# Kernel tuning notes

Measured on AMD Instinct MI355X. Metric: run time of the kernel, lower is better.

Reference implementation:

```python
import jax, jax.numpy as jnp
import numpy as np

LIS_DIM = 256
LIS_LAYERS = 3
MAX_FRAMES = 1700
MEL_DIM = 40
PET_BOOL = True
REP = 2 * LIS_DIM
B = 32
T = 1696
SCI_FACTOR = float(np.sqrt(REP / MEL_DIM)) * 20.0


def _pet():
    # sinusoidal positional encoding, exactly as Listener.compute_pet
    pos = np.arange(MAX_FRAMES, dtype=np.float64)
    d = np.arange(REP)
    ang = pos[:, None] / (10000.0 ** ((d // 2 * 2) / REP))[None, :]
    pet = np.where(d % 2 == 0, np.sin(ang), np.cos(ang)).astype(np.float32)
    return jnp.asarray(pet * np.float32(PET_BOOL))


def _lstm(x, mask, Wk, Wr, b):
    # Keras-semantics masked LSTM. x: [B,T,D], mask: [B,T] bool -> [B,T,U].
    # Gate order i, f, g(c), o as in Keras. Masked steps carry h,c (and output h).
    xz = jnp.einsum('btd,dh->bth', x, Wk) + b  # precompute input projection
    U = Wr.shape[0]

    def step(carry, inp):
        h, c = carry
        zx, m = inp  # zx: [B,4U], m: [B]
        z = zx + h @ Wr
        i, f, g, o = jnp.split(z, 4, axis=-1)
        c_new = jax.nn.sigmoid(f) * c + jax.nn.sigmoid(i) * jnp.tanh(g)
        h_new = jax.nn.sigmoid(o) * jnp.tanh(c_new)
        m = m[:, None]
        h = jnp.where(m, h_new, h)
        c = jnp.where(m, c_new, c)
        return (h, c), h

    init = (jnp.zeros((x.shape[0], U), x.dtype), jnp.zeros((x.shape[0], U), x.dtype))
    _, hs = jax.lax.scan(step, init, (xz.transpose(1, 0, 2), mask.T))
    return hs.transpose(1, 0, 2)


def _bilstm(x, mask, fk, fr, fb, bk, br, bb):
    # Keras Bidirectional(merge_mode='concat'): backward runs on time-reversed
    # input+mask, output re-reversed.
    hf = _lstm(x, mask, fk, fr, fb)
    hb = _lstm(x[:, ::-1], mask[:, ::-1], bk, br, bb)[:, ::-1]
    return jnp.concatenate([hf, hb], axis=-1)


def _forward(inputs, scale, dem_w, dem_b, layer_params, final_params, mask):
    pet = _pet()
    x = inputs @ dem_w + dem_b                       # [B,T,512]
    x = x * SCI_FACTOR * scale[0] + pet[: inputs.shape[1]]
    m = mask
    for fk, fr, fb, bk, br, bb in layer_params:
        x = _bilstm(x, m, fk, fr, fb, bk, br, bb)    # [B,t,512]
        Bb, Tt, D = x.shape
        x = x.reshape(Bb, Tt // 2, 2 * D)            # pyramid: halve time
        m = jnp.all(m.reshape(Bb, Tt // 2, 2), axis=-1)
    h = _bilstm(x, m, *final_params)                 # [B,T/8,512]
    return h, m


def setup_inputs():
    key = jax.random.key(0)
    ks = jax.random.split(key, 40)

    def w(k, shape):
        return (jax.random.normal(k, shape) * 0.08).astype(jnp.float32)

    inp = {}
    inp['inputs'] = jax.random.normal(ks[0], (B, T, MEL_DIM), jnp.float32)
    lengths = jax.random.randint(ks[1], (B,), T // 2, T + 1)
    inp['mask'] = jnp.arange(T)[None, :] < lengths[:, None]
    inp['scale'] = jnp.array([0.05], jnp.float32)
    inp['dem_w'] = w(ks[2], (MEL_DIM, REP))
    inp['dem_b'] = jnp.zeros((REP,), jnp.float32)
    dims = [REP, 4 * LIS_DIM, 4 * LIS_DIM]
    ki = 3
    for i, din in enumerate(dims):
        for pre in ('fw', 'bw'):
            inp[f'l{i}_{pre}_k'] = w(ks[ki], (din, 4 * LIS_DIM)); ki += 1
            inp[f'l{i}_{pre}_r'] = w(ks[ki], (LIS_DIM, 4 * LIS_DIM)); ki += 1
            inp[f'l{i}_{pre}_b'] = jnp.zeros((4 * LIS_DIM,), jnp.float32)
    for pre in ('fw', 'bw'):
        inp[f'f_{pre}_k'] = w(ks[ki], (4 * LIS_DIM, 4 * LIS_DIM)); ki += 1
        inp[f'f_{pre}_r'] = w(ks[ki], (LIS_DIM, 4 * LIS_DIM)); ki += 1
        inp[f'f_{pre}_b'] = jnp.zeros((4 * LIS_DIM,), jnp.float32)
    return inp


def reference(inputs, scale, dem_w, dem_b,
              l0_fw_k, l0_fw_r, l0_fw_b, l0_bw_k, l0_bw_r, l0_bw_b,
              l1_fw_k, l1_fw_r, l1_fw_b, l1_bw_k, l1_bw_r, l1_bw_b,
              l2_fw_k, l2_fw_r, l2_fw_b, l2_bw_k, l2_bw_r, l2_bw_b,
              f_fw_k, f_fw_r, f_fw_b, f_bw_k, f_bw_r, f_bw_b,
              mask):
    layer_params = [
        (l0_fw_k, l0_fw_r, l0_fw_b, l0_bw_k, l0_bw_r, l0_bw_b),
        (l1_fw_k, l1_fw_r, l1_fw_b, l1_bw_k, l1_bw_r, l1_bw_b),
        (l2_fw_k, l2_fw_r, l2_fw_b, l2_bw_k, l2_bw_r, l2_bw_b),
    ]
    final_params = (f_fw_k, f_fw_r, f_fw_b, f_bw_k, f_bw_r, f_bw_b)
    return _forward(inputs, scale, dem_w, dem_b, layer_params, final_params, mask)
```

## Files before the change

### kernel.cpp

```cpp
#include <hip/hip_runtime.h>

typedef unsigned int u32;
typedef unsigned short u16;
typedef unsigned long long u64;
typedef __attribute__((ext_vector_type(8))) short bf16x8;
typedef __attribute__((ext_vector_type(4))) float f32x4;
typedef __attribute__((ext_vector_type(4))) unsigned int u32x4;

#define MFMA16(a, b, c) __builtin_amdgcn_mfma_f32_16x16x32_bf16((a), (b), (c), 0, 0, 0)

__device__ __forceinline__ float bf2f(u16 h) {
  union { u32 u; float f; } x; x.u = ((u32)h) << 16; return x.f;
}
__device__ __forceinline__ u16 f2bf(float f) {
  union { float f; u32 u; } x; x.f = f;
  u32 r = (x.u + 0x7FFFu + ((x.u >> 16) & 1u)) >> 16;
  return (u16)r;
}
__device__ __forceinline__ float sigm(float x) { return 1.0f / (1.0f + __expf(-x)); }
__device__ __forceinline__ float tanh_(float x) {
  float e = __expf(2.0f * x);
  return 1.0f - 2.0f / (e + 1.0f);
}

__device__ __forceinline__ bool flags8_plain(const u32* p, u32 tag) {
  u32x4 a, b;
  asm volatile("global_load_dwordx4 %0, %2, off\n\t"
               "global_load_dwordx4 %1, %2, off offset:16\n\t"
               "s_waitcnt vmcnt(0)"
               : "=&v"(a), "=&v"(b) : "v"(p) : "memory");
  return (a.x == tag) & (a.y == tag) & (a.z == tag) & (a.w == tag) &
         (b.x == tag) & (b.y == tag) & (b.z == tag) & (b.w == tag);
}
__device__ __forceinline__ bool flags8_agent(const u32* p, u32 tag) {
  const u64 want = (u64)tag * 0x0000000100000001ULL;
  bool ok = true;
#pragma unroll
  for (int i = 0; i < 4; ++i)
    ok &= (__hip_atomic_load((const u64*)p + i, __ATOMIC_RELAXED,
                             __HIP_MEMORY_SCOPE_AGENT) == want);
  return ok;
}
__device__ __forceinline__ u32x4 ld16_agent(const u32* p) {
  u64 a = __hip_atomic_load((const u64*)p, __ATOMIC_RELAXED, __HIP_MEMORY_SCOPE_AGENT);
  u64 b = __hip_atomic_load((const u64*)(p + 2), __ATOMIC_RELAXED, __HIP_MEMORY_SCOPE_AGENT);
  return (u32x4){(u32)a, (u32)(a >> 32), (u32)b, (u32)(b >> 32)};
}

__global__ void sentinelK(float* __restrict__ out) {
  if (threadIdx.x == 0) out[0] = 1.0e6f;
}

__global__ void modeK(const unsigned char* __restrict__ m, int* __restrict__ mode) {
  if (threadIdx.x == 0) *mode = (m[1] | m[2]) ? 1 : 4;
}

__device__ __forceinline__ bool rawmask(const void* mp, int md, int b, int t) {
  if (md == 1) return ((const unsigned char*)mp)[b * 1696 + t] != 0;
  return ((const int*)mp)[b * 1696 + t] != 0;
}

__global__ __launch_bounds__(256) void maskK(
    const void* __restrict__ m, const int* __restrict__ mode,
    unsigned char* __restrict__ m0, unsigned char* __restrict__ m1,
    unsigned char* __restrict__ m2, unsigned char* __restrict__ m3,
    float* __restrict__ outMask) {
  int idx = blockIdx.x * 256 + threadIdx.x;
  int t = idx >> 5, b = idx & 31;
  int md = *mode;
  m0[t * 32 + b] = rawmask(m, md, b, t) ? 1 : 0;
  if (t < 848) {
    bool a = rawmask(m, md, b, 2 * t) && rawmask(m, md, b, 2 * t + 1);
    m1[t * 32 + b] = a ? 1 : 0;
  }
  if (t < 424) {
    bool a = true;
    for (int j = 0; j < 4; ++j) a = a && rawmask(m, md, b, 4 * t + j);
    m2[t * 32 + b] = a ? 1 : 0;
  }
  if (t < 212) {
    bool a = true;
    for (int j = 0; j < 8; ++j) a = a && rawmask(m, md, b, 8 * t + j);
    m3[t * 32 + b] = a ? 1 : 0;
    outMask[b * 212 + t] = a ? 1.0f : 0.0f;
  }
}

__global__ __launch_bounds__(256) void petK(float* __restrict__ pet) {
  int idx = blockIdx.x * 256 + threadIdx.x;
  int t = idx >> 9, d = idx & 511;
  double e = (double)((d >> 1) * 2) / 512.0;
  double freq = exp(e * -9.210340371976184);
  double ang = (double)t * freq;
  double vv = (d & 1) ? cos(ang) : sin(ang);
  pet[idx] = (float)vv;
}

__global__ __launch_bounds__(256) void packW(const float* __restrict__ src,
                                             u16* __restrict__ dst, int ksh, int N) {
  int idx = blockIdx.x * 256 + threadIdx.x;
  int n = idx >> ksh;
  int k = idx & ((1 << ksh) - 1);
  dst[idx] = f2bf(src[(size_t)k * N + n]);
}

__global__ void biasK(const float* __restrict__ fb, const float* __restrict__ bb,
                      float* __restrict__ dst) {
  int i = blockIdx.x * 256 + threadIdx.x;
  dst[i] = (i < 1024) ? fb[i] : bb[i - 1024];
}

__global__ __launch_bounds__(256) void x0cK(
    const float* __restrict__ inp, const float* __restrict__ dw,
    const float* __restrict__ db, const float* __restrict__ scale,
    const float* __restrict__ pet, u16* __restrict__ xc,
    int t0f, int t0b, int Cl) {
  const int bid = blockIdx.x;
  const int d = (bid >= Cl) ? 1 : 0;
  const int lt = bid - d * Cl;
  const int t = (d ? t0b : t0f) + lt;
  __shared__ float xin[32][40];
  for (int i = threadIdx.x; i < 1280; i += 256) {
    int b = i / 40, k = i - b * 40;
    xin[b][k] = inp[((size_t)b * 1696 + t) * 40 + k];
  }
  __syncthreads();
  const float sc = 71.554175279993267f * scale[0];
  for (int dd = threadIdx.x; dd < 512; dd += 256) {
    float w[40];
#pragma unroll
    for (int k = 0; k < 40; ++k) w[k] = dw[k * 512 + dd];
    const float pv = pet[t * 512 + dd];
    const float bv = db[dd];
    u16* out = xc + (((size_t)d * Cl + lt) * 32) * 512 + dd;
    for (int b = 0; b < 32; ++b) {
      float acc = bv;
#pragma unroll
      for (int k = 0; k < 40; ++k) acc += xin[b][k] * w[k];
      out[(size_t)b * 512] = f2bf(acc * sc + pv);
    }
  }
}

__device__ __forceinline__ void gemm_tile(
    u16* As, u16* Bs,
    const u16* Af, const u16* Ab, const u16* Wp, const float* bias,
    float* out, int K, int Cl, int bm, int bn, int d, int tid) {
  const u16* A = (d ? Ab : Af) + (size_t)bm * 128 * K;
  const u16* W = Wp + (size_t)d * (size_t)K * 1024 + (size_t)bn * 128 * K;
  const int wv = tid >> 6, L = tid & 63, ln = L & 15, q = L >> 4;
  const int wm = wv & 1, wn = wv >> 1;
  const int srow = L >> 3, scol = (L & 7) * 8;

  f32x4 acc[4][4];
#pragma unroll
  for (int mt = 0; mt < 4; ++mt)
#pragma unroll
    for (int nt = 0; nt < 4; ++nt) acc[mt][nt] = (f32x4){0.f, 0.f, 0.f, 0.f};

  for (int kt = 0; kt < K; kt += 64) {
#pragma unroll
    for (int j = 0; j < 4; ++j) {
      const int rg = (j * 4 + wv) * 8;
      const u16* gA = A + (size_t)(rg + srow) * K + kt + scol;
      const u16* gB = W + (size_t)(rg + srow) * K + kt + scol;
      __builtin_amdgcn_global_load_lds(
          (const __attribute__((address_space(1))) void*)gA,
          (__attribute__((address_space(3))) void*)&As[rg * 64], 16, 0, 0);
      __builtin_amdgcn_global_load_lds(
          (const __attribute__((address_space(1))) void*)gB,
          (__attribute__((address_space(3))) void*)&Bs[rg * 64], 16, 0, 0);
    }
    __syncthreads();
#pragma unroll
    for (int ks = 0; ks < 2; ++ks) {
      bf16x8 a[4], b[4];
#pragma unroll
      for (int mt = 0; mt < 4; ++mt)
        a[mt] = *(const bf16x8*)&As[(wm * 64 + mt * 16 + ln) * 64 + ks * 32 + q * 8];
#pragma unroll
      for (int nt = 0; nt < 4; ++nt)
        b[nt] = *(const bf16x8*)&Bs[(wn * 64 + nt * 16 + ln) * 64 + ks * 32 + q * 8];
#pragma unroll
      for (int mt = 0; mt < 4; ++mt)
#pragma unroll
        for (int nt = 0; nt < 4; ++nt) acc[mt][nt] = MFMA16(a[mt], b[nt], acc[mt][nt]);
    }
    __syncthreads();
  }

  float* outd = out + (size_t)d * Cl * 32768;
#pragma unroll
  for (int nt = 0; nt < 4; ++nt) {
    const int col = bn * 128 + wn * 64 + nt * 16 + ln;
    const float bv = bias[d * 1024 + col];
#pragma unroll
    for (int mt = 0; mt < 4; ++mt) {
      const int row0 = bm * 128 + wm * 64 + mt * 16 + q * 4;
#pragma unroll
      for (int r = 0; r < 4; ++r)
        outd[(size_t)(row0 + r) * 1024 + col] = acc[mt][nt][r] + bv;
    }
  }
}

__global__ __launch_bounds__(256) void gemmK(
    const u16* __restrict__ Af, const u16* __restrict__ Ab,
    const u16* __restrict__ Wp, const float* __restrict__ bias,
    float* __restrict__ out, int K, int Cl) {
  __shared__ u16 As[128 * 64];
  __shared__ u16 Bs[128 * 64];
  gemm_tile(As, Bs, Af, Ab, Wp, bias, out, K, Cl,
            blockIdx.x, blockIdx.y, blockIdx.z, threadIdx.x);
}

__global__ __launch_bounds__(256) void fusedK(
    const float* __restrict__ xzR,
    const u16* __restrict__ WrP,
    u16* __restrict__ hbufS,
    float* __restrict__ cbufL,
    int* __restrict__ flagsS,
    const unsigned char* __restrict__ msk,
    u16* __restrict__ Xnext,
    float* __restrict__ outH,
    int T, int Cl, int s0, int isFinal,
    const u16* __restrict__ Af2, const u16* __restrict__ Ab2,
    const u16* __restrict__ WpK, const float* __restrict__ biasL,
    float* __restrict__ xzW, int Kg, int Cg,
    int* __restrict__ doneL, int doneVal, int tagBase) {
  __shared__ u16 As[128 * 64];
  __shared__ u16 Bs[128 * 64];
  __shared__ u16 A_lds[32 * 264];
  __shared__ int hdone;
  __shared__ int sh_fasti;
  const int bid = blockIdx.x;
  const int tid = threadIdx.x;
  const int sub = bid & 7;
  const int grp = bid >> 3;

  if (sub == 0 && grp < 16) {
    const int rid = grp;
    const int dir = rid >> 3;
    const int wg = rid & 7;
    const int v = tid >> 6;
    const int L = tid & 63;
    const int ln = L & 15;
    const int q = L >> 4;
    const bool low = (L & 8) == 0;
    const int ug = wg * 32 + v * 8 + (L & 7);

    u32* ringB = (u32*)flagsS + dir * 128;
    u32* ringM = (u32*)flagsS + 1024 + dir * 4096;

    if (tid == 0) {
      u32 xcc = (u32)__builtin_amdgcn_s_getreg(63508) & 0xFu;
      int* chk = flagsS + 256 + ((tagBase >> 8) << 2);
      __hip_atomic_fetch_or(&chk[dir], (int)(1u << xcc), __ATOMIC_RELAXED,
                            __HIP_MEMORY_SCOPE_AGENT);
      __hip_atomic_fetch_add(&chk[2 + dir], 1, __ATOMIC_RELAXED,
                             __HIP_MEMORY_SCOPE_AGENT);
      int spins = 0;
      while (__hip_atomic_load(&chk[2 + dir], __ATOMIC_RELAXED,
                               __HIP_MEMORY_SCOPE_AGENT) < 8) {
        __builtin_amdgcn_s_sleep(2);
        if (++spins > (1 << 20)) {
          __hip_atomic_fetch_or(&chk[dir], 0x7FFFFFFF, __ATOMIC_RELAXED,
                                __HIP_MEMORY_SCOPE_AGENT);
          break;
        }
      }
      int om = __hip_atomic_load(&chk[dir], __ATOMIC_RELAXED,
                                 __HIP_MEMORY_SCOPE_AGENT);
      sh_fasti = (__popc((u32)om) == 1) ? 1 : 0;
    }
    __syncthreads();
    const bool fastp = (sh_fasti != 0);

    bf16x8 bfr[2][8];
    {
      const u16* wr = WrP + (size_t)dir * 262144;
#pragma unroll
      for (int nt = 0; nt < 2; ++nt) {
        const int n = (nt * 2 + (ln >> 3)) * 256 + ug;
#pragma unroll
        for (int ks = 0; ks < 8; ++ks)
          bfr[nt][ks] = *(const bf16x8*)(wr + (size_t)n * 256 + ks * 32 + q * 8);
      }
    }
    u16* hb = hbufS + dir * 32768;
    float* cb = cbufL + dir * 8192;

    float cst[2][4];
    if (s0 == 0) {
#pragma unroll
      for (int mt = 0; mt < 2; ++mt)
#pragma unroll
        for (int r = 0; r < 4; ++r) cst[mt][r] = 0.f;
    } else {
#pragma unroll
      for (int mt = 0; mt < 2; ++mt)
#pragma unroll
        for (int r = 0; r < 4; ++r)
          cst[mt][r] = cb[(mt * 16 + q * 4 + r) * 256 + ug];
    }

    for (int s = s0; s < s0 + Cl; ++s) {
      const int t = dir ? (T - 1 - s) : s;
      const int lt = dir ? (s0 + Cl - 1 - s) : (s - s0);
      const int ls = s - s0;

      float xzv[2][2][4];
      const float* xzt = xzR + ((size_t)dir * Cl + lt) * 32768;
#pragma unroll
      for (int nt = 0; nt < 2; ++nt) {
        const int ncol = (nt * 2 + (ln >> 3)) * 256 + ug;
#pragma unroll
        for (int mt = 0; mt < 2; ++mt)
#pragma unroll
          for (int r = 0; r < 4; ++r)
            xzv[mt][nt][r] = xzt[(size_t)(mt * 16 + q * 4 + r) * 1024 + ncol];
      }
      const u32 mk0 = *(const u32*)&msk[t * 32 + q * 4];
      const u32 mk1 = *(const u32*)&msk[t * 32 + 16 + q * 4];

      if (ls > 0) {
        if (tid == 0) {
          const u32 tg = (u32)(tagBase + ls);
          const u32* fb = ringB + ((ls - 1) & 15) * 8;
          bool got = false;
          if (fastp) {
            const u32* fm = ringM + ((ls - 1) & 31) * 128;
            for (int j = 0; j < 8; ++j) {
              if (flags8_plain(fm + j * 16, tg)) { got = true; break; }
            }
          }
          if (!got) {
            int spins = 0;
            while (!flags8_agent(fb, tg)) {
              __builtin_amdgcn_s_sleep(1);
              if (++spins > (1 << 21)) break;
            }
          }
        }
        __syncthreads();
      }

      {
        const u32* hsrc = (const u32*)(hb + ((s + 3) & 3) * 8192);
        const int m0 = tid >> 5;
        const int c4 = (tid & 31) * 4;
        const u32* p0 = hsrc + (m0)*128 + c4;
        const u32* p1 = hsrc + (8 + m0) * 128 + c4;
        const u32* p2 = hsrc + (16 + m0) * 128 + c4;
        const u32* p3 = hsrc + (24 + m0) * 128 + c4;
        u32x4 v0, v1, v2, v3;
        if (fastp) {
          v0 = *(const u32x4*)p0; v1 = *(const u32x4*)p1;
          v2 = *(const u32x4*)p2; v3 = *(const u32x4*)p3;
        } else {
          v0 = ld16_agent(p0); v1 = ld16_agent(p1);
          v2 = ld16_agent(p2); v3 = ld16_agent(p3);
        }
        const int lb = (tid & 31) * 8;
        *(u32x4*)&A_lds[(m0)*264 + lb] = v0;
        *(u32x4*)&A_lds[(8 + m0) * 264 + lb] = v1;
        *(u32x4*)&A_lds[(16 + m0) * 264 + lb] = v2;
        *(u32x4*)&A_lds[(24 + m0) * 264 + lb] = v3;
      }
      __syncthreads();

      f32x4 acc[2][2];
#pragma unroll
      for (int mt = 0; mt < 2; ++mt)
#pragma unroll
        for (int nt = 0; nt < 2; ++nt) acc[mt][nt] = (f32x4){0.f, 0.f, 0.f, 0.f};
#pragma unroll
      for (int ks = 0; ks < 8; ++ks) {
        bf16x8 a0 = *(const bf16x8*)&A_lds[ln * 264 + ks * 32 + q * 8];
        bf16x8 a1 = *(const bf16x8*)&A_lds[(16 + ln) * 264 + ks * 32 + q * 8];
        acc[0][0] = MFMA16(a0, bfr[0][ks], acc[0][0]);
        acc[0][1] = MFMA16(a0, bfr[1][ks], acc[0][1]);
        acc[1][0] = MFMA16(a1, bfr[0][ks], acc[1][0]);
        acc[1][1] = MFMA16(a1, bfr[1][ks], acc[1][1]);
      }

      float hsv[2][4];
#pragma unroll
      for (int mt = 0; mt < 2; ++mt) {
        const u32 mkw = mt ? mk1 : mk0;
#pragma unroll
        for (int r = 0; r < 4; ++r) {
          float z0 = acc[mt][0][r] + xzv[mt][0][r];
          float z1 = acc[mt][1][r] + xzv[mt][1][r];
          float z0p = __shfl_xor(z0, 8);
          float z1p = __shfl_xor(z1, 8);
          float iv = low ? z0 : z0p;
          float fv = low ? z0p : z0;
          float gv = low ? z1 : z1p;
          float ov = low ? z1p : z1;
          float cold = cst[mt][r];
          float cn = sigm(fv) * cold + sigm(iv) * tanh_(gv);
          float hn = sigm(ov) * tanh_(cn);
          const int m = mt * 16 + q * 4 + r;
          float hold = bf2f(A_lds[m * 264 + ug]);
          bool mb = ((mkw >> (8 * r)) & 0xffu) != 0;
          cst[mt][r] = mb ? cn : cold;
          float hs = mb ? hn : hold;
          hsv[mt][r] = hs;
        }
      }

      {
        u32* hdst = (u32*)(hb + (s & 3) * 8192);
#pragma unroll
        for (int mt = 0; mt < 2; ++mt) {
#pragma unroll
          for (int r = 0; r < 4; ++r) {
            u32 lo = (u32)f2bf(hsv[mt][r]);
            u32 par = (u32)__shfl_xor((int)lo, 1);
            u32 val = lo | (par << 16);
            if (low && ((ln & 1) == 0)) {
              const int m = mt * 16 + q * 4 + r;
              if (fastp)
                hdst[m * 128 + (ug >> 1)] = val;
              else
                __hip_atomic_store(&hdst[m * 128 + (ug >> 1)], val,
                                   __ATOMIC_RELAXED, __HIP_MEMORY_SCOPE_AGENT);
            }
          }
        }
      }

      asm volatile("s_waitcnt vmcnt(0)" ::: "memory");
      __syncthreads();
      if (tid == 0) {
        const u32 tg = (u32)(tagBase + ls + 1);
        if (fastp) {
          u32* mir = ringM + (ls & 31) * 128 + wg;
#pragma unroll
          for (int j = 0; j < 8; ++j)
            asm volatile("global_store_dword %0, %1, off" ::"v"(mir + j * 16),
                         "v"(tg) : "memory");
        }
        __hip_atomic_store(ringB + (ls & 15) * 8 + wg, tg, __ATOMIC_RELAXED,
                           __HIP_MEMORY_SCOPE_AGENT);
      }

      if (low) {
#pragma unroll
        for (int mt = 0; mt < 2; ++mt)
#pragma unroll
          for (int r = 0; r < 4; ++r) {
            const int m = mt * 16 + q * 4 + r;
            if (isFinal)
              outH[((size_t)m * T + t) * 512 + dir * 256 + ug] = hsv[mt][r];
            else
              Xnext[((size_t)(t >> 1) * 32 + m) * 1024 + (t & 1) * 512 + dir * 256 + ug] =
                  f2bf(hsv[mt][r]);
          }
      }
    }

    if (low) {
#pragma unroll
      for (int mt = 0; mt < 2; ++mt)
#pragma unroll
        for (int r = 0; r < 4; ++r)
          cb[(mt * 16 + q * 4 + r) * 256 + ug] = cst[mt][r];
    }
    if (wg == 0 && tid == 0)
      __hip_atomic_store(&doneL[dir * 16], doneVal, __ATOMIC_RELAXED,
                         __HIP_MEMORY_SCOPE_AGENT);
  } else {
    const int gidx = (bid < 128) ? (grp * 7 + sub - 1) : (112 + (bid - 128));
    if (Cg > 0) {
      const int nM = Cg >> 2;
      const int total = nM * 16;
      for (int tt = gidx; tt < total; tt += 240) {
        const int d = tt / (nM * 8);
        const int r2 = tt - d * (nM * 8);
        const int bn = r2 / nM;
        const int bm = r2 - bn * nM;
        gemm_tile(As, Bs, Af2, Ab2, WpK, biasL, xzW, Kg, Cg, bm, bn, d, tid);
      }
    }
    if (tid == 0) hdone = 0;
    __syncthreads();
    float hx = 1.0f + (float)tid * 1.0e-6f;
    const float ha = 1.0000001f, hc = 1.0e-7f;
    for (int it = 0; it < (1 << 16); ++it) {
#pragma unroll 64
      for (int i = 0; i < 512; ++i)
        asm volatile("v_fmac_f32 %0, %1, %2" : "+v"(hx) : "v"(ha), "v"(hc));
      if (tid == 0) {
        int d0 = __hip_atomic_load(&doneL[0],  __ATOMIC_RELAXED, __HIP_MEMORY_SCOPE_AGENT);
        int d1 = __hip_atomic_load(&doneL[16], __ATOMIC_RELAXED, __HIP_MEMORY_SCOPE_AGENT);
        if (d0 >= doneVal && d1 >= doneVal) hdone = 1;
      }
      __syncthreads();
      if (hdone) break;
      __syncthreads();
    }
    if (hx == 1.2345e-37f) ((volatile float*)doneL)[8] = hx;
  }
}

extern "C" void kernel_launch(void* const* d_in, const int* in_sizes, int n_in,
                              void* d_out, int out_size, void* d_ws, size_t ws_size,
                              hipStream_t stream) {
  char* ws = (char*)d_ws;
  constexpr size_t O_PET   = 0;
  constexpr size_t O_WK    = 3473408;
  constexpr size_t O_BIAS  = O_WK + 14680064;
  constexpr size_t O_WR    = O_BIAS + 32768;
  constexpr size_t O_M0    = O_WR + 4194304;
  constexpr size_t O_M1    = O_M0 + 54272;
  constexpr size_t O_M2    = O_M1 + 27136;
  constexpr size_t O_M3    = O_M2 + 13568;
  constexpr size_t O_MODE  = O_M3 + 6784;
  constexpr size_t O_FLAGS = O_MODE + 256;
  constexpr size_t O_DONE  = O_FLAGS + 54272;
  constexpr size_t O_HBUF  = O_DONE + 512;
  constexpr size_t O_CBUF  = O_HBUF + 262144;
  constexpr size_t O_XB0   = O_CBUF + 262144;
  constexpr size_t O_XB1   = O_XB0 + 55574528;
  constexpr size_t O_XC    = O_XB1 + 27787264;

  int C = 0;
  if      (ws_size >= O_XC + 212ull * 589824) C = 212;
  else if (ws_size >= O_XC + 106ull * 589824) C = 106;
  else if (ws_size >= O_XC + 53ull * 589824)  C = 53;
  if (C == 0) { sentinelK<<<1, 64, 0, stream>>>((float*)d_out); return; }

  hipMemsetAsync(ws + O_FLAGS, 0, 54272 + 512 + 131072, stream);

  modeK<<<1, 64, 0, stream>>>((const unsigned char*)d_in[1], (int*)(ws + O_MODE));
  maskK<<<212, 256, 0, stream>>>(d_in[1], (const int*)(ws + O_MODE),
                                 (unsigned char*)(ws + O_M0), (unsigned char*)(ws + O_M1),
                                 (unsigned char*)(ws + O_M2), (unsigned char*)(ws + O_M3),
                                 (float*)d_out + 3473408);
  petK<<<3392, 256, 0, stream>>>((float*)(ws + O_PET));

  u16* wk = (u16*)(ws + O_WK);
  u16* wrp = (u16*)(ws + O_WR);
  float* bias = (float*)(ws + O_BIAS);
  packW<<<2048, 256, 0, stream>>>((const float*)d_in[5],  wk + 0,       9, 1024);
  packW<<<2048, 256, 0, stream>>>((const float*)d_in[8],  wk + 524288,  9, 1024);
  packW<<<4096, 256, 0, stream>>>((const float*)d_in[11], wk + 1048576, 10, 1024);
  packW<<<4096, 256, 0, stream>>>((const float*)d_in[14], wk + 2097152, 10, 1024);
  packW<<<4096, 256, 0, stream>>>((const float*)d_in[17], wk + 3145728, 10, 1024);
  packW<<<4096, 256, 0, stream>>>((const float*)d_in[20], wk + 4194304, 10, 1024);
  packW<<<4096, 256, 0, stream>>>((const float*)d_in[23], wk + 5242880, 10, 1024);
  packW<<<4096, 256, 0, stream>>>((const float*)d_in[26], wk + 6291456, 10, 1024);
  packW<<<1024, 256, 0, stream>>>((const float*)d_in[6],  wrp + 0,       8, 1024);
  packW<<<1024, 256, 0, stream>>>((const float*)d_in[9],  wrp + 262144,  8, 1024);
  packW<<<1024, 256, 0, stream>>>((const float*)d_in[12], wrp + 524288,  8, 1024);
  packW<<<1024, 256, 0, stream>>>((const float*)d_in[15], wrp + 786432,  8, 1024);
  packW<<<1024, 256, 0, stream>>>((const float*)d_in[18], wrp + 1048576, 8, 1024);
  packW<<<1024, 256, 0, stream>>>((const float*)d_in[21], wrp + 1310720, 8, 1024);
  packW<<<1024, 256, 0, stream>>>((const float*)d_in[24], wrp + 1572864, 8, 1024);
  packW<<<1024, 256, 0, stream>>>((const float*)d_in[27], wrp + 1835008, 8, 1024);
  biasK<<<8, 256, 0, stream>>>((const float*)d_in[7],  (const float*)d_in[10], bias + 0);
  biasK<<<8, 256, 0, stream>>>((const float*)d_in[13], (const float*)d_in[16], bias + 2048);
  biasK<<<8, 256, 0, stream>>>((const float*)d_in[19], (const float*)d_in[22], bias + 4096);
  biasK<<<8, 256, 0, stream>>>((const float*)d_in[25], (const float*)d_in[28], bias + 6144);

  u16* XB0 = (u16*)(ws + O_XB0);
  u16* XB1 = (u16*)(ws + O_XB1);
  u16* xc  = (u16*)(ws + O_XC);
  float* xzp[2] = {(float*)(ws + O_XC + (size_t)C * 65536),
                   (float*)(ws + O_XC + (size_t)C * 65536 + (size_t)C * 262144)};
  int* flags = (int*)(ws + O_FLAGS);
  int* done  = (int*)(ws + O_DONE);
  u16* hbuf = (u16*)(ws + O_HBUF);
  float* cbuf = (float*)(ws + O_CBUF);
  unsigned char* masks[4] = {
      (unsigned char*)(ws + O_M0), (unsigned char*)(ws + O_M1),
      (unsigned char*)(ws + O_M2), (unsigned char*)(ws + O_M3)};

  const int    Ts[4]    = {1696, 848, 424, 212};
  const int    Ks[4]    = {512, 1024, 1024, 1024};
  const size_t wkOff[4] = {0, 1048576, 3145728, 5242880};
  const size_t wrOff[4] = {0, 524288, 1048576, 1572864};
  const int    bOff[4]  = {0, 2048, 4096, 6144};
  u16* Xin[4]  = {nullptr, XB0, XB1, XB0};
  u16* Xout[4] = {XB0, XB1, XB0, nullptr};

  int launchIdx = 0;
  for (int l = 0; l < 4; ++l) {
    const int T = Ts[l], K = Ks[l];
    const int Cl = (C < T) ? C : T;
    const int R = T / Cl;

    if (l > 0)
      hipMemsetAsync(ws + O_HBUF, 0, 131072, stream);

    const u16 *Af, *Ab;
    if (l == 0) {
      x0cK<<<2 * Cl, 256, 0, stream>>>((const float*)d_in[0], (const float*)d_in[3],
                                       (const float*)d_in[4], (const float*)d_in[2],
                                       (const float*)(ws + O_PET), xc, 0, T - Cl, Cl);
      Af = xc; Ab = xc + (size_t)Cl * 16384;
    } else {
      Af = Xin[l]; Ab = Xin[l] + (size_t)(T - Cl) * 32768;
    }
    gemmK<<<dim3(Cl / 4, 8, 2), 256, 0, stream>>>(
        Af, Ab, wk + wkOff[l], bias + bOff[l], xzp[0], K, Cl);

    for (int r = 0; r < R; ++r) {
      const int hasN = (r + 1 < R);
      const u16 *Af2 = nullptr, *Ab2 = nullptr;
      if (hasN) {
        if (l == 0) {
          x0cK<<<2 * Cl, 256, 0, stream>>>((const float*)d_in[0], (const float*)d_in[3],
                                           (const float*)d_in[4], (const float*)d_in[2],
                                           (const float*)(ws + O_PET), xc,
                                           (r + 1) * Cl, T - (r + 2) * Cl, Cl);
          Af2 = xc; Ab2 = xc + (size_t)Cl * 16384;
        } else {
          Af2 = Xin[l] + (size_t)(r + 1) * Cl * 32768;
          Ab2 = Xin[l] + (size_t)(T - (r + 2) * Cl) * 32768;
        }
      }
      fusedK<<<256, 256, 0, stream>>>(
          xzp[r & 1], wrp + wrOff[l], hbuf,
          cbuf + (size_t)l * 16384, flags, masks[l], Xout[l],
          (l == 3) ? (float*)d_out : nullptr, T, Cl, r * Cl, (l == 3) ? 1 : 0,
          Af2, Ab2, wk + wkOff[l], bias + bOff[l], xzp[(r + 1) & 1], K,
          hasN ? Cl : 0, done + (size_t)l * 32, r + 1, launchIdx << 8);
      ++launchIdx;
    }
  }
}
```

Before: 12.82 ms.

## Halve recurrent LSTM workgroups per direction and read h directly into MFMA fragments

The recurrent part of the fused kernel now uses 4 workgroups per direction instead of 8. Each workgroup owns 64 hidden units and all four gates, which removes the cross-lane shuffles used for gate exchange and cuts the per-step inter-workgroup flag polling. The previous hidden state is loaded straight from global memory into MFMA A-fragments, skipping the LDS staging copy and one barrier. The next step's xz and mask values are prefetched into double-buffered registers, and output stores are shifted onto waves 1-3. The cost is twice as much recurrent weight held in registers per thread, more per-workgroup compute on the serial path, and a relocated mirror flag ring inside the h buffer.

```diff
diff --git a/kernel.cpp b/kernel.cpp
--- a/kernel.cpp
+++ b/kernel.cpp
@@ -23,20 +23,17 @@
   return 1.0f - 2.0f / (e + 1.0f);
 }
 
-__device__ __forceinline__ bool flags8_plain(const u32* p, u32 tag) {
-  u32x4 a, b;
-  asm volatile("global_load_dwordx4 %0, %2, off\n\t"
-               "global_load_dwordx4 %1, %2, off offset:16\n\t"
-               "s_waitcnt vmcnt(0)"
-               : "=&v"(a), "=&v"(b) : "v"(p) : "memory");
-  return (a.x == tag) & (a.y == tag) & (a.z == tag) & (a.w == tag) &
-         (b.x == tag) & (b.y == tag) & (b.z == tag) & (b.w == tag);
-}
-__device__ __forceinline__ bool flags8_agent(const u32* p, u32 tag) {
+__device__ __forceinline__ bool probe4(const u32* p, u32 tag) {
+  u32x4 a;
+  asm volatile("global_load_dwordx4 %0, %1, off\n\ts_waitcnt vmcnt(0)"
+               : "=&v"(a) : "v"(p) : "memory");
+  return (a.x == tag) & (a.y == tag) & (a.z == tag) & (a.w == tag);
+}
+__device__ __forceinline__ bool flags4_agent(const u32* p, u32 tag) {
   const u64 want = (u64)tag * 0x0000000100000001ULL;
   bool ok = true;
 #pragma unroll
-  for (int i = 0; i < 4; ++i)
+  for (int i = 0; i < 2; ++i)
     ok &= (__hip_atomic_load((const u64*)p + i, __ATOMIC_RELAXED,
                              __HIP_MEMORY_SCOPE_AGENT) == want);
   return ok;
@@ -230,7 +227,7 @@
     int* __restrict__ doneL, int doneVal, int tagBase) {
   __shared__ u16 As[128 * 64];
   __shared__ u16 Bs[128 * 64];
-  __shared__ u16 A_lds[32 * 264];
+  __shared__ float w0h[64][8];
   __shared__ int hdone;
   __shared__ int sh_fasti;
   const int bid = blockIdx.x;
@@ -238,30 +235,29 @@
   const int sub = bid & 7;
   const int grp = bid >> 3;
 
-  if (sub == 0 && grp < 16) {
+  if (sub == 0 && grp < 8) {
     const int rid = grp;
-    const int dir = rid >> 3;
-    const int wg = rid & 7;
+    const int dir = rid >> 2;
+    const int wg = rid & 3;
     const int v = tid >> 6;
     const int L = tid & 63;
     const int ln = L & 15;
     const int q = L >> 4;
-    const bool low = (L & 8) == 0;
-    const int ug = wg * 32 + v * 8 + (L & 7);
-
-    u32* ringB = (u32*)flagsS + dir * 128;
-    u32* ringM = (u32*)flagsS + 1024 + dir * 4096;
+    const int ug = wg * 64 + v * 16 + ln;
+
+    u32* ringB = (u32*)flagsS + dir * 64;
+    u32* ringM = (u32*)(hbufS + 65536) + dir * 8192;
 
     if (tid == 0) {
       u32 xcc = (u32)__builtin_amdgcn_s_getreg(63508) & 0xFu;
-      int* chk = flagsS + 256 + ((tagBase >> 8) << 2);
+      int* chk = flagsS + 128 + ((tagBase >> 8) << 2);
       __hip_atomic_fetch_or(&chk[dir], (int)(1u << xcc), __ATOMIC_RELAXED,
                             __HIP_MEMORY_SCOPE_AGENT);
       __hip_atomic_fetch_add(&chk[2 + dir], 1, __ATOMIC_RELAXED,
                              __HIP_MEMORY_SCOPE_AGENT);
       int spins = 0;
       while (__hip_atomic_load(&chk[2 + dir], __ATOMIC_RELAXED,
-                               __HIP_MEMORY_SCOPE_AGENT) < 8) {
+                               __HIP_MEMORY_SCOPE_AGENT) < 4) {
         __builtin_amdgcn_s_sleep(2);
         if (++spins > (1 << 20)) {
           __hip_atomic_fetch_or(&chk[dir], 0x7FFFFFFF, __ATOMIC_RELAXED,
@@ -276,12 +272,12 @@
     __syncthreads();
     const bool fastp = (sh_fasti != 0);
 
-    bf16x8 bfr[2][8];
+    bf16x8 bfr[4][8];
     {
       const u16* wr = WrP + (size_t)dir * 262144;
 #pragma unroll
-      for (int nt = 0; nt < 2; ++nt) {
-        const int n = (nt * 2 + (ln >> 3)) * 256 + ug;
+      for (int nt = 0; nt < 4; ++nt) {
+        const int n = nt * 256 + ug;
 #pragma unroll
         for (int ks = 0; ks < 8; ++ks)
           bfr[nt][ks] = *(const bf16x8*)(wr + (size_t)n * 256 + ks * 32 + q * 8);
@@ -304,39 +300,43 @@
           cst[mt][r] = cb[(mt * 16 + q * 4 + r) * 256 + ug];
     }
 
-    for (int s = s0; s < s0 + Cl; ++s) {
+    float xzA[2][4][4], xzB[2][4][4];
+    u32 mkA0, mkA1, mkB0, mkB1;
+
+    auto prefetch = [&](int ss, float (&xz)[2][4][4], u32& k0, u32& k1) {
+      const int ssc = (ss < s0 + Cl) ? ss : (s0 + Cl - 1);
+      const int tt = dir ? (T - 1 - ssc) : ssc;
+      const int ltt = dir ? (s0 + Cl - 1 - ssc) : (ssc - s0);
+      const float* xzt = xzR + ((size_t)dir * Cl + ltt) * 32768;
+#pragma unroll
+      for (int nt = 0; nt < 4; ++nt)
+#pragma unroll
+        for (int mt = 0; mt < 2; ++mt)
+#pragma unroll
+          for (int r = 0; r < 4; ++r)
+            xz[mt][nt][r] = xzt[(size_t)(mt * 16 + q * 4 + r) * 1024 + nt * 256 + ug];
+      k0 = *(const u32*)&msk[tt * 32 + q * 4];
+      k1 = *(const u32*)&msk[tt * 32 + 16 + q * 4];
+    };
+
+    auto step = [&](int s, float (&xzC)[2][4][4], u32 mkC0, u32 mkC1,
+                    float (&xzN)[2][4][4], u32& mkN0, u32& mkN1) {
       const int t = dir ? (T - 1 - s) : s;
-      const int lt = dir ? (s0 + Cl - 1 - s) : (s - s0);
       const int ls = s - s0;
-
-      float xzv[2][2][4];
-      const float* xzt = xzR + ((size_t)dir * Cl + lt) * 32768;
-#pragma unroll
-      for (int nt = 0; nt < 2; ++nt) {
-        const int ncol = (nt * 2 + (ln >> 3)) * 256 + ug;
-#pragma unroll
-        for (int mt = 0; mt < 2; ++mt)
-#pragma unroll
-          for (int r = 0; r < 4; ++r)
-            xzv[mt][nt][r] = xzt[(size_t)(mt * 16 + q * 4 + r) * 1024 + ncol];
-      }
-      const u32 mk0 = *(const u32*)&msk[t * 32 + q * 4];
-      const u32 mk1 = *(const u32*)&msk[t * 32 + 16 + q * 4];
 
       if (ls > 0) {
         if (tid == 0) {
           const u32 tg = (u32)(tagBase + ls);
-          const u32* fb = ringB + ((ls - 1) & 15) * 8;
+          const u32* fb = ringB + ((ls - 1) & 15) * 4;
           bool got = false;
           if (fastp) {
-            const u32* fm = ringM + ((ls - 1) & 31) * 128;
-            for (int j = 0; j < 8; ++j) {
-              if (flags8_plain(fm + j * 16, tg)) { got = true; break; }
-            }
+            const u32* fm = ringM + ((ls - 1) & 31) * 256;
+            for (int j = 0; j < 8; ++j)
+              if (probe4(fm + j * 32, tg)) { got = true; break; }
           }
           if (!got) {
             int spins = 0;
-            while (!flags8_agent(fb, tg)) {
+            while (!flags4_agent(fb, tg)) {
               __builtin_amdgcn_s_sleep(1);
               if (++spins > (1 << 21)) break;
             }
@@ -345,108 +345,118 @@
         __syncthreads();
       }
 
-      {
-        const u32* hsrc = (const u32*)(hb + ((s + 3) & 3) * 8192);
-        const int m0 = tid >> 5;
-        const int c4 = (tid & 31) * 4;
-        const u32* p0 = hsrc + (m0)*128 + c4;
-        const u32* p1 = hsrc + (8 + m0) * 128 + c4;
-        const u32* p2 = hsrc + (16 + m0) * 128 + c4;
-        const u32* p3 = hsrc + (24 + m0) * 128 + c4;
-        u32x4 v0, v1, v2, v3;
-        if (fastp) {
-          v0 = *(const u32x4*)p0; v1 = *(const u32x4*)p1;
-          v2 = *(const u32x4*)p2; v3 = *(const u32x4*)p3;
-        } else {
-          v0 = ld16_agent(p0); v1 = ld16_agent(p1);
-          v2 = ld16_agent(p2); v3 = ld16_agent(p3);
-        }
-        const int lb = (tid & 31) * 8;
-        *(u32x4*)&A_lds[(m0)*264 + lb] = v0;
-        *(u32x4*)&A_lds[(8 + m0) * 264 + lb] = v1;
-        *(u32x4*)&A_lds[(16 + m0) * 264 + lb] = v2;
-        *(u32x4*)&A_lds[(24 + m0) * 264 + lb] = v3;
-      }
-      __syncthreads();
-
-      f32x4 acc[2][2];
+      const u16* hsrc = hb + ((s + 3) & 3) * 8192;
+      bf16x8 af0[8], af1[8];
+      float holdv[2][4];
+      if (fastp) {
+#pragma unroll
+        for (int ks = 0; ks < 8; ++ks) {
+          af0[ks] = *(const bf16x8*)(hsrc + ln * 256 + ks * 32 + q * 8);
+          af1[ks] = *(const bf16x8*)(hsrc + (16 + ln) * 256 + ks * 32 + q * 8);
+        }
+#pragma unroll
+        for (int mt = 0; mt < 2; ++mt)
+#pragma unroll
+          for (int r = 0; r < 4; ++r)
+            holdv[mt][r] = bf2f(hsrc[(mt * 16 + q * 4 + r) * 256 + ug]);
+      } else {
+#pragma unroll
+        for (int ks = 0; ks < 8; ++ks) {
+          u32x4 t0 = ld16_agent((const u32*)(hsrc + ln * 256 + ks * 32 + q * 8));
+          u32x4 t1 = ld16_agent((const u32*)(hsrc + (16 + ln) * 256 + ks * 32 + q * 8));
+          af0[ks] = *(bf16x8*)&t0;
+          af1[ks] = *(bf16x8*)&t1;
+        }
+#pragma unroll
+        for (int mt = 0; mt < 2; ++mt)
+#pragma unroll
+          for (int r = 0; r < 4; ++r) {
+            const int ix = (mt * 16 + q * 4 + r) * 256 + ug;
+            u32 w = __hip_atomic_load((const u32*)hsrc + (ix >> 1), __ATOMIC_RELAXED,
+                                      __HIP_MEMORY_SCOPE_AGENT);
+            holdv[mt][r] = bf2f((u16)((ix & 1) ? (w >> 16) : (w & 0xffffu)));
+          }
+      }
+
+      prefetch(s + 1, xzN, mkN0, mkN1);
+
+      f32x4 acc[2][4];
 #pragma unroll
       for (int mt = 0; mt < 2; ++mt)
 #pragma unroll
-        for (int nt = 0; nt < 2; ++nt) acc[mt][nt] = (f32x4){0.f, 0.f, 0.f, 0.f};
-#pragma unroll
-      for (int ks = 0; ks < 8; ++ks) {
-        bf16x8 a0 = *(const bf16x8*)&A_lds[ln * 264 + ks * 32 + q * 8];
-        bf16x8 a1 = *(const bf16x8*)&A_lds[(16 + ln) * 264 + ks * 32 + q * 8];
-        acc[0][0] = MFMA16(a0, bfr[0][ks], acc[0][0]);
-        acc[0][1] = MFMA16(a0, bfr[1][ks], acc[0][1]);
-        acc[1][0] = MFMA16(a1, bfr[0][ks], acc[1][0]);
-        acc[1][1] = MFMA16(a1, bfr[1][ks], acc[1][1]);
-      }
-
-      float hsv[2][4];
+        for (int nt = 0; nt < 4; ++nt) acc[mt][nt] = (f32x4){0.f, 0.f, 0.f, 0.f};
+#pragma unroll
+      for (int ks = 0; ks < 8; ++ks)
+#pragma unroll
+        for (int nt = 0; nt < 4; ++nt) {
+          acc[0][nt] = MFMA16(af0[ks], bfr[nt][ks], acc[0][nt]);
+          acc[1][nt] = MFMA16(af1[ks], bfr[nt][ks], acc[1][nt]);
+        }
+
+      float hsv[2][4]; u16 hsu[2][4];
 #pragma unroll
       for (int mt = 0; mt < 2; ++mt) {
-        const u32 mkw = mt ? mk1 : mk0;
+        const u32 mkw = mt ? mkC1 : mkC0;
 #pragma unroll
         for (int r = 0; r < 4; ++r) {
-          float z0 = acc[mt][0][r] + xzv[mt][0][r];
-          float z1 = acc[mt][1][r] + xzv[mt][1][r];
-          float z0p = __shfl_xor(z0, 8);
-          float z1p = __shfl_xor(z1, 8);
-          float iv = low ? z0 : z0p;
-          float fv = low ? z0p : z0;
-          float gv = low ? z1 : z1p;
-          float ov = low ? z1p : z1;
+          float iv = acc[mt][0][r] + xzC[mt][0][r];
+          float fv = acc[mt][1][r] + xzC[mt][1][r];
+          float gv = acc[mt][2][r] + xzC[mt][2][r];
+          float ov = acc[mt][3][r] + xzC[mt][3][r];
           float cold = cst[mt][r];
           float cn = sigm(fv) * cold + sigm(iv) * tanh_(gv);
           float hn = sigm(ov) * tanh_(cn);
-          const int m = mt * 16 + q * 4 + r;
-          float hold = bf2f(A_lds[m * 264 + ug]);
           bool mb = ((mkw >> (8 * r)) & 0xffu) != 0;
           cst[mt][r] = mb ? cn : cold;
-          float hs = mb ? hn : hold;
-          hsv[mt][r] = hs;
-        }
-      }
-
-      {
-        u32* hdst = (u32*)(hb + (s & 3) * 8192);
-#pragma unroll
-        for (int mt = 0; mt < 2; ++mt) {
+          float hs = mb ? hn : holdv[mt][r];
+          hsv[mt][r] = hs; hsu[mt][r] = f2bf(hs);
+        }
+      }
+
+      if (v == 0) {
+        *(f32x4*)&w0h[L][0] = (f32x4){hsv[0][0], hsv[0][1], hsv[0][2], hsv[0][3]};
+        *(f32x4*)&w0h[L][4] = (f32x4){hsv[1][0], hsv[1][1], hsv[1][2], hsv[1][3]};
+      }
+
+      u16* hdst = hb + (s & 3) * 8192;
+      if (fastp) {
+#pragma unroll
+        for (int mt = 0; mt < 2; ++mt)
+#pragma unroll
+          for (int r = 0; r < 4; ++r)
+            hdst[(mt * 16 + q * 4 + r) * 256 + ug] = hsu[mt][r];
+      } else {
+#pragma unroll
+        for (int mt = 0; mt < 2; ++mt)
 #pragma unroll
           for (int r = 0; r < 4; ++r) {
-            u32 lo = (u32)f2bf(hsv[mt][r]);
+            u32 lo = (u32)hsu[mt][r];
             u32 par = (u32)__shfl_xor((int)lo, 1);
-            u32 val = lo | (par << 16);
-            if (low && ((ln & 1) == 0)) {
-              const int m = mt * 16 + q * 4 + r;
-              if (fastp)
-                hdst[m * 128 + (ug >> 1)] = val;
-              else
-                __hip_atomic_store(&hdst[m * 128 + (ug >> 1)], val,
-                                   __ATOMIC_RELAXED, __HIP_MEMORY_SCOPE_AGENT);
+            if ((ln & 1) == 0) {
+              const int ix = (mt * 16 + q * 4 + r) * 256 + ug;
+              __hip_atomic_store((u32*)hdst + (ix >> 1), lo | (par << 16),
+                                 __ATOMIC_RELAXED, __HIP_MEMORY_SCOPE_AGENT);
             }
           }
-        }
       }
 
       asm volatile("s_waitcnt vmcnt(0)" ::: "memory");
       __syncthreads();
-      if (tid == 0) {
+
+      if (tid == 64) {
         const u32 tg = (u32)(tagBase + ls + 1);
         if (fastp) {
-          u32* mir = ringM + (ls & 31) * 128 + wg;
+          u32* mir = ringM + (ls & 31) * 256 + wg;
 #pragma unroll
           for (int j = 0; j < 8; ++j)
-            asm volatile("global_store_dword %0, %1, off" ::"v"(mir + j * 16),
+            asm volatile("global_store_dword %0, %1, off" ::"v"(mir + j * 32),
                          "v"(tg) : "memory");
         }
-        __hip_atomic_store(ringB + (ls & 15) * 8 + wg, tg, __ATOMIC_RELAXED,
+        __hip_atomic_store(ringB + (ls & 15) * 4 + wg, tg, __ATOMIC_RELAXED,
                            __HIP_MEMORY_SCOPE_AGENT);
       }
 
-      if (low) {
+      if (v != 0) {
 #pragma unroll
         for (int mt = 0; mt < 2; ++mt)
 #pragma unroll
@@ -456,27 +466,46 @@
               outH[((size_t)m * T + t) * 512 + dir * 256 + ug] = hsv[mt][r];
             else
               Xnext[((size_t)(t >> 1) * 32 + m) * 1024 + (t & 1) * 512 + dir * 256 + ug] =
-                  f2bf(hsv[mt][r]);
+                  hsu[mt][r];
           }
       }
-    }
-
-    if (low) {
-#pragma unroll
-      for (int mt = 0; mt < 2; ++mt)
-#pragma unroll
-        for (int r = 0; r < 4; ++r)
-          cb[(mt * 16 + q * 4 + r) * 256 + ug] = cst[mt][r];
-    }
+      if (v == 1) {
+        const int u0 = wg * 64 + ln;
+#pragma unroll
+        for (int mt = 0; mt < 2; ++mt)
+#pragma unroll
+          for (int r = 0; r < 4; ++r) {
+            const int m = mt * 16 + q * 4 + r;
+            float hv = w0h[L][mt * 4 + r];
+            if (isFinal)
+              outH[((size_t)m * T + t) * 512 + dir * 256 + u0] = hv;
+            else
+              Xnext[((size_t)(t >> 1) * 32 + m) * 1024 + (t & 1) * 512 + dir * 256 + u0] =
+                  f2bf(hv);
+          }
+      }
+    };
+
+    prefetch(s0, xzA, mkA0, mkA1);
+    for (int s = s0; s < s0 + Cl; s += 2) {
+      step(s, xzA, mkA0, mkA1, xzB, mkB0, mkB1);
+      if (s + 1 < s0 + Cl) step(s + 1, xzB, mkB0, mkB1, xzA, mkA0, mkA1);
+    }
+
+#pragma unroll
+    for (int mt = 0; mt < 2; ++mt)
+#pragma unroll
+      for (int r = 0; r < 4; ++r)
+        cb[(mt * 16 + q * 4 + r) * 256 + ug] = cst[mt][r];
     if (wg == 0 && tid == 0)
       __hip_atomic_store(&doneL[dir * 16], doneVal, __ATOMIC_RELAXED,
                          __HIP_MEMORY_SCOPE_AGENT);
   } else {
-    const int gidx = (bid < 128) ? (grp * 7 + sub - 1) : (112 + (bid - 128));
+    const int gidx = (sub > 0) ? (grp * 7 + sub - 1) : (224 + (grp - 8));
     if (Cg > 0) {
       const int nM = Cg >> 2;
       const int total = nM * 16;
-      for (int tt = gidx; tt < total; tt += 240) {
+      for (int tt = gidx; tt < total; tt += 248) {
         const int d = tt / (nM * 8);
         const int r2 = tt - d * (nM * 8);
         const int bn = r2 / nM;
@@ -532,7 +561,7 @@
   else if (ws_size >= O_XC + 53ull * 589824)  C = 53;
   if (C == 0) { sentinelK<<<1, 64, 0, stream>>>((float*)d_out); return; }
 
-  hipMemsetAsync(ws + O_FLAGS, 0, 54272 + 512 + 131072, stream);
+  hipMemsetAsync(ws + O_FLAGS, 0, 54272 + 512 + 262144, stream);
 
   modeK<<<1, 64, 0, stream>>>((const unsigned char*)d_in[1], (int*)(ws + O_MODE));
   maskK<<<212, 256, 0, stream>>>(d_in[1], (const int*)(ws + O_MODE),
```

Measured after the change: 17.24 ms. 1.34x slower.

## Move flag mirror ring into hbuf region, defer xz loads, offload output stores

Applied to the files above, without the earlier changes.

Relocates the per-step mirror flag ring from the flags area into the space after the h buffers, widening its stride, and clears the larger region with the memset. The xz and mask loads move after the flag wait. Output stores move from the low lanes, which compute h, onto the idle high lanes, with wave 0's values relayed through a small LDS array. The flag-posting thread also changes from thread 0 to a thread in another wave. Together these aim to shorten the serial critical path of each recurrent step, but the deferred loads may expose their latency after the wait.

```diff
diff --git a/kernel.cpp b/kernel.cpp
--- a/kernel.cpp
+++ b/kernel.cpp
@@ -231,6 +231,7 @@
   __shared__ u16 As[128 * 64];
   __shared__ u16 Bs[128 * 64];
   __shared__ u16 A_lds[32 * 264];
+  __shared__ float w0h[32][8];
   __shared__ int hdone;
   __shared__ int sh_fasti;
   const int bid = blockIdx.x;
@@ -250,7 +251,7 @@
     const int ug = wg * 32 + v * 8 + (L & 7);
 
     u32* ringB = (u32*)flagsS + dir * 128;
-    u32* ringM = (u32*)flagsS + 1024 + dir * 4096;
+    u32* ringM = (u32*)(hbufS + 65536) + dir * 8192;
 
     if (tid == 0) {
       u32 xcc = (u32)__builtin_amdgcn_s_getreg(63508) & 0xFu;
@@ -309,30 +310,15 @@
       const int lt = dir ? (s0 + Cl - 1 - s) : (s - s0);
       const int ls = s - s0;
 
-      float xzv[2][2][4];
-      const float* xzt = xzR + ((size_t)dir * Cl + lt) * 32768;
-#pragma unroll
-      for (int nt = 0; nt < 2; ++nt) {
-        const int ncol = (nt * 2 + (ln >> 3)) * 256 + ug;
-#pragma unroll
-        for (int mt = 0; mt < 2; ++mt)
-#pragma unroll
-          for (int r = 0; r < 4; ++r)
-            xzv[mt][nt][r] = xzt[(size_t)(mt * 16 + q * 4 + r) * 1024 + ncol];
-      }
-      const u32 mk0 = *(const u32*)&msk[t * 32 + q * 4];
-      const u32 mk1 = *(const u32*)&msk[t * 32 + 16 + q * 4];
-
       if (ls > 0) {
         if (tid == 0) {
           const u32 tg = (u32)(tagBase + ls);
           const u32* fb = ringB + ((ls - 1) & 15) * 8;
           bool got = false;
           if (fastp) {
-            const u32* fm = ringM + ((ls - 1) & 31) * 128;
-            for (int j = 0; j < 8; ++j) {
-              if (flags8_plain(fm + j * 16, tg)) { got = true; break; }
-            }
+            const u32* fm = ringM + ((ls - 1) & 31) * 256;
+            for (int j = 0; j < 8; ++j)
+              if (flags8_plain(fm + j * 32, tg)) { got = true; break; }
           }
           if (!got) {
             int spins = 0;
@@ -344,6 +330,22 @@
         }
         __syncthreads();
       }
+
+      float xzv[2][2][4];
+      {
+        const float* xzt = xzR + ((size_t)dir * Cl + lt) * 32768;
+#pragma unroll
+        for (int nt = 0; nt < 2; ++nt) {
+          const int ncol = (nt * 2 + (ln >> 3)) * 256 + ug;
+#pragma unroll
+          for (int mt = 0; mt < 2; ++mt)
+#pragma unroll
+            for (int r = 0; r < 4; ++r)
+              xzv[mt][nt][r] = xzt[(size_t)(mt * 16 + q * 4 + r) * 1024 + ncol];
+        }
+      }
+      const u32 mk0 = *(const u32*)&msk[t * 32 + q * 4];
+      const u32 mk1 = *(const u32*)&msk[t * 32 + 16 + q * 4];
 
       {
         const u32* hsrc = (const u32*)(hb + ((s + 3) & 3) * 8192);
@@ -410,6 +412,14 @@
         }
       }
 
+      if (v == 0 && low) {
+        const int widx = q * 8 + (L & 7);
+#pragma unroll
+        for (int mt = 0; mt < 2; ++mt)
+#pragma unroll
+          for (int r = 0; r < 4; ++r) w0h[widx][mt * 4 + r] = hsv[mt][r];
+      }
+
       {
         u32* hdst = (u32*)(hb + (s & 3) * 8192);
 #pragma unroll
@@ -433,20 +443,21 @@
 
       asm volatile("s_waitcnt vmcnt(0)" ::: "memory");
       __syncthreads();
-      if (tid == 0) {
+
+      if (tid == 72) {
         const u32 tg = (u32)(tagBase + ls + 1);
         if (fastp) {
-          u32* mir = ringM + (ls & 31) * 128 + wg;
+          u32* mir = ringM + (ls & 31) * 256 + wg;
 #pragma unroll
           for (int j = 0; j < 8; ++j)
-            asm volatile("global_store_dword %0, %1, off" ::"v"(mir + j * 16),
+            asm volatile("global_store_dword %0, %1, off" ::"v"(mir + j * 32),
                          "v"(tg) : "memory");
         }
         __hip_atomic_store(ringB + (ls & 15) * 8 + wg, tg, __ATOMIC_RELAXED,
                            __HIP_MEMORY_SCOPE_AGENT);
       }
 
-      if (low) {
+      if (!low && v != 0) {
 #pragma unroll
         for (int mt = 0; mt < 2; ++mt)
 #pragma unroll
@@ -457,6 +468,22 @@
             else
               Xnext[((size_t)(t >> 1) * 32 + m) * 1024 + (t & 1) * 512 + dir * 256 + ug] =
                   f2bf(hsv[mt][r]);
+          }
+      }
+      if (!low && v == 1) {
+        const int widx = q * 8 + (L & 7);
+        const int u0 = wg * 32 + (L & 7);
+#pragma unroll
+        for (int mt = 0; mt < 2; ++mt)
+#pragma unroll
+          for (int r = 0; r < 4; ++r) {
+            const int m = mt * 16 + q * 4 + r;
+            float hv = w0h[widx][mt * 4 + r];
+            if (isFinal)
+              outH[((size_t)m * T + t) * 512 + dir * 256 + u0] = hv;
+            else
+              Xnext[((size_t)(t >> 1) * 32 + m) * 1024 + (t & 1) * 512 + dir * 256 + u0] =
+                  f2bf(hv);
           }
       }
     }
@@ -532,7 +559,7 @@
   else if (ws_size >= O_XC + 53ull * 589824)  C = 53;
   if (C == 0) { sentinelK<<<1, 64, 0, stream>>>((float*)d_out); return; }
 
-  hipMemsetAsync(ws + O_FLAGS, 0, 54272 + 512 + 131072, stream);
+  hipMemsetAsync(ws + O_FLAGS, 0, 54272 + 512 + 262144, stream);
 
   modeK<<<1, 64, 0, stream>>>((const unsigned char*)d_in[1], (int*)(ws + O_MODE));
   maskK<<<212, 256, 0, stream>>>(d_in[1], (const int*)(ws + O_MODE),
```

Result: slower. 13.31 ms (+3.8%).
